# Performance work log

Measured on AMD Instinct MI355X. Metric: run time of the kernel, lower is better.

## Reference

```python
import jax, jax.numpy as jnp
import numpy as np

S1 = 2048      # seqx1_dim
S2 = 2048      # seqx2_dim
E1 = 1024      # seqx1_emb_dim
E2 = 1024      # seqx2_emb_dim
U = 1024       # units
M = E1 + E2    # margex_dim
B = 2048
TAU = 0.5


def setup_inputs() -> dict:
    key = jax.random.key(0)
    ks = jax.random.split(key, 20)
    g = lambda k, shp, fan: jax.random.normal(k, shp, jnp.float32) * (1.0 / np.sqrt(fan))
    bias = jnp.zeros((4 * U,), jnp.float32).at[U:2 * U].set(1.0)  # unit_forget_bias
    return {
        'inputs': jax.random.normal(ks[0], (B, S1 + S2), jnp.float32),
        'h_tm1': jax.random.normal(ks[1], (B, U), jnp.float32),
        'c_tm1': jax.random.normal(ks[2], (B, U), jnp.float32),
        'crohis_tm': jax.random.normal(ks[3], (B, M), jnp.float32),
        'embed_w1': g(ks[4], (S1, E1), S1),
        'embed_w2': g(ks[5], (S2, E2), S2),
        'w12_w': g(ks[6], (E1, E1), E1),
        'w12_u': g(ks[7], (E2, E1), E2),
        'w12_v': g(ks[8], (E2, E1), E2),
        'w21_w': g(ks[9], (E2, E2), E2),
        'w21_u': g(ks[10], (E1, E2), E1),
        'w21_v': g(ks[11], (E1, E2), E1),
        'crohis_w': g(ks[12], (M, U), M),
        'crohis_b': jnp.zeros((U,), jnp.float32),
        'decomp_w': g(ks[13], (M, M), M),
        'decomp_b': jnp.zeros((M,), jnp.float32),
        'kernel': g(ks[14], (M, 4 * U), M),
        'recurrent_kernel': g(ks[15], (U, 4 * U), U),
        'bias': bias,
    }


def _cell(inputs, h_tm1, c_tm1, crohis_tm, embed_w1, embed_w2, w12_w, w12_u, w12_v,
          w21_w, w21_u, w21_v, crohis_w, crohis_b, decomp_w, decomp_b,
          kernel, recurrent_kernel, bias):
    seqx1 = inputs[:, :S1]
    seqx2 = inputs[:, S1:]
    e1 = seqx1 @ embed_w1                                   # [B,E1]
    e2 = seqx2 @ embed_w2                                   # [B,E2]
    # dual cross-attention gates (softmax over feature axis, as K.softmax default)
    ca12 = jax.nn.softmax(jnp.tanh(e1 @ w12_w + e2 @ w12_u) * (e2 @ w12_v), axis=-1)
    ca21 = jax.nn.softmax(jnp.tanh(e2 @ w21_w + e1 @ w21_u) * (e1 @ w21_v), axis=-1)
    x = jnp.concatenate([e1 * ca12, e2 * ca21], axis=-1)    # [B,M]
    # cross-history decomposition gate and decayed merge
    decomp = jax.nn.sigmoid(crohis_tm @ decomp_w + decomp_b)
    crohis = TAU * crohis_tm * decomp + (1.0 - TAU) * x     # [B,M]
    h_cro = jnp.tanh(crohis @ crohis_w + crohis_b)          # [B,U]
    # fused LSTM (implementation=2)
    z = x @ kernel + h_tm1 @ recurrent_kernel + bias        # [B,4U]
    zi, zf, zc, zo = jnp.split(z, 4, axis=-1)
    i = jax.nn.sigmoid(zi)
    f = jax.nn.sigmoid(zf)
    c = f * c_tm1 + i * jnp.tanh(zc)
    o = jax.nn.sigmoid(zo)
    h = o * jnp.tanh(c) + h_cro
    return h, c, crohis


def reference(inputs, h_tm1, c_tm1, crohis_tm, embed_w1, embed_w2, w12_w, w12_u, w12_v,
              w21_w, w21_u, w21_v, crohis_w, crohis_b, decomp_w, decomp_b,
              kernel, recurrent_kernel, bias):
    return _cell(inputs, h_tm1, c_tm1, crohis_tm, embed_w1, embed_w2, w12_w, w12_u,
                 w12_v, w21_w, w21_u, w21_v, crohis_w, crohis_b, decomp_w, decomp_b,
                 kernel, recurrent_kernel, bias)
```

## Files before the change

### kernel.cpp

```cpp
#include <hip/hip_runtime.h>
#include <stdint.h>

typedef unsigned short u16;
typedef __bf16 bf16x8 __attribute__((ext_vector_type(8)));
typedef float f32x4 __attribute__((ext_vector_type(4)));
typedef u16 u16x8 __attribute__((ext_vector_type(8)));

__device__ __forceinline__ u16 bf16_bits(float f) {
  uint32_t x = __float_as_uint(f);
  uint32_t r = (x + 0x7FFFu + ((x >> 16) & 1u)) >> 16;
  return (u16)r;
}
__device__ __forceinline__ float bits_f32(u16 u) {
  return __uint_as_float(((uint32_t)u) << 16);
}
__device__ __forceinline__ float sigm(float x) { return 1.f / (1.f + expf(-x)); }

__device__ __forceinline__ void gload_lds16(const void* g, void* l) {
  __builtin_amdgcn_global_load_lds(
      (const __attribute__((address_space(1))) void*)g,
      (__attribute__((address_space(3))) void*)l,
      16, 0, 0);
}

__global__ __launch_bounds__(256) void cvt_all_kernel(
    const float* __restrict__ inp, const float* __restrict__ ctm,
    const float* __restrict__ h, u16* __restrict__ bf_in,
    u16* __restrict__ bf_ctm, u16* __restrict__ xh) {
  int i = blockIdx.x * 256 + threadIdx.x;
  const float* src;
  u16* dst;
  if (i < 1048576) {
    src = inp + (size_t)i * 8;
    dst = bf_in + (size_t)i * 8;
  } else if (i < 1048576 + 524288) {
    int j = i - 1048576;
    src = ctm + (size_t)j * 8;
    dst = bf_ctm + (size_t)j * 8;
  } else {
    int j = i - 1572864;
    int row = j >> 7;
    int c0 = (j & 127) << 3;
    src = h + (size_t)row * 1024 + c0;
    dst = xh + (size_t)row * 3072 + 2048 + c0;
  }
  const f32x4* s = (const f32x4*)src;
  f32x4 a = s[0], b = s[1];
  u16x8 o;
#pragma unroll
  for (int k = 0; k < 4; ++k) { o[k] = bf16_bits(a[k]); o[4 + k] = bf16_bits(b[k]); }
  *(u16x8*)dst = o;
}

struct TransGroups {
  const float* src[12];
  u16* dst[12];
  int N[12];
  int ld[12];
  long long off[12];
  int start[13];
};

__global__ __launch_bounds__(256) void transpose_all_kernel(TransGroups tg) {
  __shared__ float t[32][33];
  int bid = blockIdx.x;
  int g = 0;
#pragma unroll
  for (int i = 1; i < 12; ++i)
    if (bid >= tg.start[i]) g = i;
  int local = bid - tg.start[g];
  const float* src = tg.src[g];
  u16* dst = tg.dst[g];
  int N = tg.N[g];
  int ld = tg.ld[g];
  long long off = tg.off[g];
  int ntx = N >> 5;
  int n0 = (local % ntx) << 5;
  int k0 = (local / ntx) << 5;
  int tx = threadIdx.x & 31, ty = threadIdx.x >> 5;
#pragma unroll
  for (int r = ty; r < 32; r += 8) t[r][tx] = src[(size_t)(k0 + r) * N + n0 + tx];
  __syncthreads();
#pragma unroll
  for (int r = ty; r < 32; r += 8)
    dst[off + (size_t)(n0 + r) * ld + k0 + tx] = bf16_bits(t[tx][r]);
}

enum { EPI_F32 = 0, EPI_BF16 = 1, EPI_DHALF = 2, EPI_TANH = 3 };

struct GemmGroups {
  const u16* A[4];
  const u16* Bt[4];
  float* C[4];
  u16* Cb[4];
  const float* bias[4];
  const float* aux[4];
  int lda[4];
  int K[4];
  int nbx[4];
  int ldc[4];
  int ldcb[4];
  int epi[4];
  int start[4];
};

__global__ __launch_bounds__(256) void gemm_grouped(GemmGroups gg) {
  __shared__ u16 As[128 * 32];
  __shared__ u16 Bs[128 * 32];
  const int bid = blockIdx.x;
  int g = 0;
#pragma unroll
  for (int i = 1; i < 4; ++i)
    if (bid >= gg.start[i]) g = i;
  const int local = bid - gg.start[g];
  const u16* __restrict__ A = gg.A[g];
  const u16* __restrict__ Bt = gg.Bt[g];
  const int lda = gg.lda[g];
  const int K = gg.K[g];
  const int nbx = gg.nbx[g];

  const int tid = threadIdx.x;
  const int lane = tid & 63;
  const int wid = tid >> 6;
  const int wr = wid >> 1, wc = wid & 1;
  const int brow = (local / nbx) * 128;
  const int bcol = (local % nbx) * 128;

  f32x4 acc[4][4] = {};

  const int s0 = wid, s1 = wid + 4;
  const int oA0 = s0 * 1024 + lane * 16;
  const int oA1 = s1 * 1024 + lane * 16;

  const int nk = K >> 5;
  for (int kt = 0; kt < nk; ++kt) {
    __syncthreads();
    {
      const char* gp;
      int o = oA0;
      gp = (const char*)A + (((size_t)(brow + (o >> 6)) * lda) << 1) + (kt << 6) + (o & 63);
      gload_lds16(gp, (char*)As + s0 * 1024);
      o = oA1;
      gp = (const char*)A + (((size_t)(brow + (o >> 6)) * lda) << 1) + (kt << 6) + (o & 63);
      gload_lds16(gp, (char*)As + s1 * 1024);
      o = oA0;
      gp = (const char*)Bt + (((size_t)(bcol + (o >> 6)) * K) << 1) + (kt << 6) + (o & 63);
      gload_lds16(gp, (char*)Bs + s0 * 1024);
      o = oA1;
      gp = (const char*)Bt + (((size_t)(bcol + (o >> 6)) * K) << 1) + (kt << 6) + (o & 63);
      gload_lds16(gp, (char*)Bs + s1 * 1024);
    }
    __syncthreads();

    bf16x8 af[4], bf[4];
#pragma unroll
    for (int m = 0; m < 4; ++m) {
      int r = wr * 64 + m * 16 + (lane & 15);
      af[m] = *(const bf16x8*)((const char*)As + r * 64 + ((lane >> 4) << 4));
    }
#pragma unroll
    for (int n = 0; n < 4; ++n) {
      int cidx = wc * 64 + n * 16 + (lane & 15);
      bf[n] = *(const bf16x8*)((const char*)Bs + cidx * 64 + ((lane >> 4) << 4));
    }
#pragma unroll
    for (int m = 0; m < 4; ++m)
#pragma unroll
      for (int n = 0; n < 4; ++n)
        acc[m][n] = __builtin_amdgcn_mfma_f32_16x16x32_bf16(af[m], bf[n], acc[m][n], 0, 0, 0);
  }

  float* __restrict__ C = gg.C[g];
  u16* __restrict__ Cb = gg.Cb[g];
  const float* __restrict__ bias = gg.bias[g];
  const float* __restrict__ aux = gg.aux[g];
  const int ldc = gg.ldc[g];
  const int ldcb = gg.ldcb[g];
  const int epi = gg.epi[g];

  const int r0 = brow + wr * 64 + ((lane >> 4) << 2);
  const int c0 = bcol + wc * 64 + (lane & 15);
#pragma unroll
  for (int m = 0; m < 4; ++m) {
#pragma unroll
    for (int n = 0; n < 4; ++n) {
#pragma unroll
      for (int j = 0; j < 4; ++j) {
        int gr = r0 + m * 16 + j;
        int gc = c0 + n * 16;
        float v = acc[m][n][j];
        if (epi == EPI_F32) {
          C[(size_t)gr * ldc + gc] = v;
        } else if (epi == EPI_BF16) {
          Cb[(size_t)gr * ldcb + gc] = bf16_bits(v);
        } else if (epi == EPI_DHALF) {
          size_t ci = (size_t)gr * ldc + gc;
          C[ci] = 0.5f * aux[ci] * sigm(v + bias[gc]);
        } else {
          C[(size_t)gr * ldc + gc] = tanhf(v + bias[gc]);
        }
      }
    }
  }
}

__global__ __launch_bounds__(256) void softmax_cro_kernel(
    const float* __restrict__ T_ALL, const u16* __restrict__ E_B,
    const float* __restrict__ DCRO, u16* __restrict__ XH_B,
    float* __restrict__ out_cro, u16* __restrict__ CRO_B) {
  __shared__ float smx[4], sms[4];
  int row = blockIdx.x >> 1;
  int half = blockIdx.x & 1;
  const float* T = T_ALL + (size_t)row * 4096 + half * 1024;
  const float* V = T_ALL + (size_t)row * 4096 + 2048 + half * 1024;
  int tid = threadIdx.x;
  float s[4];
  float lmax = -1e30f;
#pragma unroll
  for (int i = 0; i < 4; ++i) {
    int c = tid + (i << 8);
    s[i] = tanhf(T[c]) * V[c];
    lmax = fmaxf(lmax, s[i]);
  }
#pragma unroll
  for (int o = 32; o; o >>= 1) lmax = fmaxf(lmax, __shfl_xor(lmax, o, 64));
  if ((tid & 63) == 0) smx[tid >> 6] = lmax;
  __syncthreads();
  float bmax = fmaxf(fmaxf(smx[0], smx[1]), fmaxf(smx[2], smx[3]));
  float lsum = 0.f;
#pragma unroll
  for (int i = 0; i < 4; ++i) { s[i] = expf(s[i] - bmax); lsum += s[i]; }
#pragma unroll
  for (int o = 32; o; o >>= 1) lsum += __shfl_xor(lsum, o, 64);
  if ((tid & 63) == 0) sms[tid >> 6] = lsum;
  __syncthreads();
  float inv = 1.f / (sms[0] + sms[1] + sms[2] + sms[3]);
#pragma unroll
  for (int i = 0; i < 4; ++i) {
    int c = tid + (i << 8);
    int col = half * 1024 + c;
    size_t mi = (size_t)row * 2048 + col;
    float x = bits_f32(E_B[mi]) * s[i] * inv;
    XH_B[(size_t)row * 3072 + col] = bf16_bits(x);
    float cro = DCRO[mi] + 0.5f * x;
    out_cro[mi] = cro;
    CRO_B[mi] = bf16_bits(cro);
  }
}

__global__ __launch_bounds__(256) void gates_kernel(
    const float* __restrict__ Z, const float* __restrict__ bias,
    const float* __restrict__ c_tm1, const float* __restrict__ hcro,
    float* __restrict__ out_h, float* __restrict__ out_c) {
  int i = blockIdx.x * 256 + threadIdx.x;
  int row = i >> 8;
  int u0 = (i & 255) << 2;
  const float* zr = Z + (size_t)row * 4096;
  f32x4 zi = *(const f32x4*)(zr + u0);
  f32x4 zf = *(const f32x4*)(zr + 1024 + u0);
  f32x4 zc = *(const f32x4*)(zr + 2048 + u0);
  f32x4 zo = *(const f32x4*)(zr + 3072 + u0);
  f32x4 bi = *(const f32x4*)(bias + u0);
  f32x4 bff = *(const f32x4*)(bias + 1024 + u0);
  f32x4 bc = *(const f32x4*)(bias + 2048 + u0);
  f32x4 bo = *(const f32x4*)(bias + 3072 + u0);
  f32x4 ct = *(const f32x4*)(c_tm1 + (size_t)row * 1024 + u0);
  f32x4 hc = *(const f32x4*)(hcro + (size_t)row * 1024 + u0);
  f32x4 h, c;
#pragma unroll
  for (int k = 0; k < 4; ++k) {
    float I = sigm(zi[k] + bi[k]);
    float F = sigm(zf[k] + bff[k]);
    float O = sigm(zo[k] + bo[k]);
    float cc = F * ct[k] + I * tanhf(zc[k] + bc[k]);
    c[k] = cc;
    h[k] = O * tanhf(cc) + hc[k];
  }
  *(f32x4*)(out_h + (size_t)row * 1024 + u0) = h;
  *(f32x4*)(out_c + (size_t)row * 1024 + u0) = c;
}

extern "C" void kernel_launch(void* const* d_in, const int* in_sizes, int n_in,
                              void* d_out, int out_size, void* d_ws, size_t ws_size,
                              hipStream_t stream) {
  const float* in_inputs = (const float*)d_in[0];
  const float* in_h      = (const float*)d_in[1];
  const float* in_c      = (const float*)d_in[2];
  const float* in_ctm    = (const float*)d_in[3];
  const float* w_e1      = (const float*)d_in[4];
  const float* w_e2      = (const float*)d_in[5];
  const float* w12w      = (const float*)d_in[6];
  const float* w12u      = (const float*)d_in[7];
  const float* w12v      = (const float*)d_in[8];
  const float* w21w      = (const float*)d_in[9];
  const float* w21u      = (const float*)d_in[10];
  const float* w21v      = (const float*)d_in[11];
  const float* w_cro     = (const float*)d_in[12];
  const float* b_cro     = (const float*)d_in[13];
  const float* w_dec     = (const float*)d_in[14];
  const float* b_dec     = (const float*)d_in[15];
  const float* w_k       = (const float*)d_in[16];
  const float* w_rk      = (const float*)d_in[17];
  const float* b_z       = (const float*)d_in[18];

  float* out_h   = (float*)d_out;
  float* out_c   = out_h + (size_t)2048 * 1024;
  float* out_cro = out_h + (size_t)2 * 2048 * 1024;

  char* ws = (char*)d_ws;
  size_t off = 0;
  auto alloc = [&](size_t bytes) {
    char* p = ws + off;
    off += (bytes + 255) & ~(size_t)255;
    return p;
  };
  u16* BF_IN    = (u16*)alloc((size_t)2048 * 4096 * 2);
  u16* BF_CROTM = (u16*)alloc((size_t)2048 * 2048 * 2);
  u16* E_B      = (u16*)alloc((size_t)2048 * 2048 * 2);
  float* T_ALL  = (float*)alloc((size_t)2048 * 4096 * 4);
  float* DCRO   = (float*)alloc((size_t)2048 * 2048 * 4);
  u16* XH_B     = (u16*)alloc((size_t)2048 * 3072 * 2);
  u16* CRO_B    = (u16*)alloc((size_t)2048 * 2048 * 2);
  float* HCRO   = (float*)alloc((size_t)2048 * 1024 * 4);
  u16* WT_E1    = (u16*)alloc((size_t)1024 * 2048 * 2);
  u16* WT_E2    = (u16*)alloc((size_t)1024 * 2048 * 2);
  u16* WT_T     = (u16*)alloc((size_t)2048 * 2048 * 2);
  u16* WT_V12   = (u16*)alloc((size_t)1024 * 1024 * 2);
  u16* WT_V21   = (u16*)alloc((size_t)1024 * 1024 * 2);
  u16* WT_CRO   = (u16*)alloc((size_t)1024 * 2048 * 2);
  u16* WT_DEC   = (u16*)alloc((size_t)2048 * 2048 * 2);
  u16* WT_KRK   = (u16*)alloc((size_t)4096 * 3072 * 2);
  float* Z = T_ALL;

  const int INF = 0x7fffffff;

  cvt_all_kernel<<<7168, 256, 0, stream>>>(in_inputs, in_ctm, in_h, BF_IN, BF_CROTM, XH_B);

  {
    TransGroups tg;
    int s = 0, gi = 0;
    auto add = [&](const float* src, int K, int N, u16* dst, int ld, long long dOff) {
      tg.src[gi] = src; tg.dst[gi] = dst; tg.N[gi] = N; tg.ld[gi] = ld; tg.off[gi] = dOff;
      tg.start[gi] = s; s += (K >> 5) * (N >> 5); ++gi;
    };
    add(w_e1, 2048, 1024, WT_E1, 2048, 0);
    add(w_e2, 2048, 1024, WT_E2, 2048, 0);
    add(w12w, 1024, 1024, WT_T, 2048, 0);
    add(w12u, 1024, 1024, WT_T, 2048, 1024);
    add(w21u, 1024, 1024, WT_T, 2048, (long long)1024 * 2048);
    add(w21w, 1024, 1024, WT_T, 2048, (long long)1024 * 2048 + 1024);
    add(w12v, 1024, 1024, WT_V12, 1024, 0);
    add(w21v, 1024, 1024, WT_V21, 1024, 0);
    add(w_cro, 2048, 1024, WT_CRO, 2048, 0);
    add(w_dec, 2048, 2048, WT_DEC, 2048, 0);
    add(w_k, 2048, 4096, WT_KRK, 3072, 0);
    add(w_rk, 1024, 4096, WT_KRK, 3072, 2048);
    tg.start[12] = s;
    transpose_all_kernel<<<s, 256, 0, stream>>>(tg);
  }

  auto mkgrp = [&]() {
    GemmGroups gg;
    for (int i = 0; i < 4; ++i) {
      gg.A[i] = nullptr; gg.Bt[i] = nullptr; gg.C[i] = nullptr; gg.Cb[i] = nullptr;
      gg.bias[i] = nullptr; gg.aux[i] = nullptr;
      gg.lda[i] = 0; gg.K[i] = 32; gg.nbx[i] = 1; gg.ldc[i] = 0; gg.ldcb[i] = 0;
      gg.epi[i] = EPI_F32; gg.start[i] = INF;
    }
    return gg;
  };

  {
    GemmGroups gg = mkgrp();
    gg.A[0] = BF_CROTM; gg.Bt[0] = WT_DEC; gg.lda[0] = 2048; gg.K[0] = 2048;
    gg.nbx[0] = 16; gg.C[0] = DCRO; gg.ldc[0] = 2048; gg.epi[0] = EPI_DHALF;
    gg.bias[0] = b_dec; gg.aux[0] = in_ctm; gg.start[0] = 0;
    gg.A[1] = BF_IN; gg.Bt[1] = WT_E1; gg.lda[1] = 4096; gg.K[1] = 2048;
    gg.nbx[1] = 8; gg.Cb[1] = E_B; gg.ldcb[1] = 2048; gg.epi[1] = EPI_BF16;
    gg.start[1] = 256;
    gg.A[2] = BF_IN + 2048; gg.Bt[2] = WT_E2; gg.lda[2] = 4096; gg.K[2] = 2048;
    gg.nbx[2] = 8; gg.Cb[2] = E_B + 1024; gg.ldcb[2] = 2048; gg.epi[2] = EPI_BF16;
    gg.start[2] = 384;
    gemm_grouped<<<512, 256, 0, stream>>>(gg);
  }

  {
    GemmGroups gg = mkgrp();
    gg.A[0] = E_B; gg.Bt[0] = WT_T; gg.lda[0] = 2048; gg.K[0] = 2048;
    gg.nbx[0] = 16; gg.C[0] = T_ALL; gg.ldc[0] = 4096; gg.epi[0] = EPI_F32;
    gg.start[0] = 0;
    gg.A[1] = E_B + 1024; gg.Bt[1] = WT_V12; gg.lda[1] = 2048; gg.K[1] = 1024;
    gg.nbx[1] = 8; gg.C[1] = T_ALL + 2048; gg.ldc[1] = 4096; gg.epi[1] = EPI_F32;
    gg.start[1] = 256;
    gg.A[2] = E_B; gg.Bt[2] = WT_V21; gg.lda[2] = 2048; gg.K[2] = 1024;
    gg.nbx[2] = 8; gg.C[2] = T_ALL + 3072; gg.ldc[2] = 4096; gg.epi[2] = EPI_F32;
    gg.start[2] = 384;
    gemm_grouped<<<512, 256, 0, stream>>>(gg);
  }

  softmax_cro_kernel<<<4096, 256, 0, stream>>>(T_ALL, E_B, DCRO, XH_B, out_cro, CRO_B);

  {
    GemmGroups gg = mkgrp();
    gg.A[0] = XH_B; gg.Bt[0] = WT_KRK; gg.lda[0] = 3072; gg.K[0] = 3072;
    gg.nbx[0] = 32; gg.C[0] = Z; gg.ldc[0] = 4096; gg.epi[0] = EPI_F32;
    gg.start[0] = 0;
    gg.A[1] = CRO_B; gg.Bt[1] = WT_CRO; gg.lda[1] = 2048; gg.K[1] = 2048;
    gg.nbx[1] = 8; gg.C[1] = HCRO; gg.ldc[1] = 1024; gg.epi[1] = EPI_TANH;
    gg.bias[1] = b_cro; gg.start[1] = 512;
    gemm_grouped<<<640, 256, 0, stream>>>(gg);
  }

  gates_kernel<<<2048, 256, 0, stream>>>(Z, b_z, in_c, HCRO, out_h, out_c);
}
```

Measured before the change: 519.6 us.

## Double-buffer GEMM LDS tiles and widen transpose tiles to packed bf16 stores

The grouped GEMM now uses two LDS buffers and issues the global-to-LDS loads for the next K tile before computing on the current one. This removes one barrier per iteration and lets memory latency overlap the MFMA work. The weight transpose kernel now handles 64x32 tiles and writes pairs of bf16 values as 32-bit stores, which halves the block count and widens the writes. The cost is double the LDS footprint, which may reduce occupancy, plus one redundant prefetch on the last iteration.

```diff
diff --git a/kernel.cpp b/kernel.cpp
--- a/kernel.cpp
+++ b/kernel.cpp
@@ -62,7 +62,7 @@
 };
 
 __global__ __launch_bounds__(256) void transpose_all_kernel(TransGroups tg) {
-  __shared__ float t[32][33];
+  __shared__ float t[64][33];
   int bid = blockIdx.x;
   int g = 0;
 #pragma unroll
@@ -74,16 +74,19 @@
   int N = tg.N[g];
   int ld = tg.ld[g];
   long long off = tg.off[g];
-  int ntx = N >> 5;
-  int n0 = (local % ntx) << 5;
-  int k0 = (local / ntx) << 5;
+  int ntn = N >> 5;
+  int n0 = (local % ntn) << 5;
+  int k0 = (local / ntn) << 6;
   int tx = threadIdx.x & 31, ty = threadIdx.x >> 5;
 #pragma unroll
-  for (int r = ty; r < 32; r += 8) t[r][tx] = src[(size_t)(k0 + r) * N + n0 + tx];
+  for (int r = ty; r < 64; r += 8) t[r][tx] = src[(size_t)(k0 + r) * N + n0 + tx];
   __syncthreads();
 #pragma unroll
-  for (int r = ty; r < 32; r += 8)
-    dst[off + (size_t)(n0 + r) * ld + k0 + tx] = bf16_bits(t[tx][r]);
+  for (int j = ty; j < 32; j += 8) {
+    uint32_t lo = bf16_bits(t[2 * tx][j]);
+    uint32_t hi = bf16_bits(t[2 * tx + 1][j]);
+    *(uint32_t*)(&dst[off + (size_t)(n0 + j) * ld + k0 + 2 * tx]) = lo | (hi << 16);
+  }
 }
 
 enum { EPI_F32 = 0, EPI_BF16 = 1, EPI_DHALF = 2, EPI_TANH = 3 };
@@ -105,8 +108,8 @@
 };
 
 __global__ __launch_bounds__(256) void gemm_grouped(GemmGroups gg) {
-  __shared__ u16 As[128 * 32];
-  __shared__ u16 Bs[128 * 32];
+  __shared__ u16 As[2][4096];
+  __shared__ u16 Bs[2][4096];
   const int bid = blockIdx.x;
   int g = 0;
 #pragma unroll
@@ -132,43 +135,50 @@
   const int oA0 = s0 * 1024 + lane * 16;
   const int oA1 = s1 * 1024 + lane * 16;
 
+  const char* gA0 = (const char*)A + (((size_t)(brow + (oA0 >> 6)) * lda) << 1) + (oA0 & 63);
+  const char* gA1 = (const char*)A + (((size_t)(brow + (oA1 >> 6)) * lda) << 1) + (oA1 & 63);
+  const char* gB0 = (const char*)Bt + (((size_t)(bcol + (oA0 >> 6)) * K) << 1) + (oA0 & 63);
+  const char* gB1 = (const char*)Bt + (((size_t)(bcol + (oA1 >> 6)) * K) << 1) + (oA1 & 63);
+
+#define STAGE(buf, koff)                                              \
+  {                                                                   \
+    gload_lds16(gA0 + (koff), (char*)As + (buf) * 8192 + s0 * 1024);  \
+    gload_lds16(gA1 + (koff), (char*)As + (buf) * 8192 + s1 * 1024);  \
+    gload_lds16(gB0 + (koff), (char*)Bs + (buf) * 8192 + s0 * 1024);  \
+    gload_lds16(gB1 + (koff), (char*)Bs + (buf) * 8192 + s1 * 1024);  \
+  }
+
   const int nk = K >> 5;
+  STAGE(0, 0);
+  __syncthreads();
+  int cur = 0;
   for (int kt = 0; kt < nk; ++kt) {
-    __syncthreads();
-    {
-      const char* gp;
-      int o = oA0;
-      gp = (const char*)A + (((size_t)(brow + (o >> 6)) * lda) << 1) + (kt << 6) + (o & 63);
-      gload_lds16(gp, (char*)As + s0 * 1024);
-      o = oA1;
-      gp = (const char*)A + (((size_t)(brow + (o >> 6)) * lda) << 1) + (kt << 6) + (o & 63);
-      gload_lds16(gp, (char*)As + s1 * 1024);
-      o = oA0;
-      gp = (const char*)Bt + (((size_t)(bcol + (o >> 6)) * K) << 1) + (kt << 6) + (o & 63);
-      gload_lds16(gp, (char*)Bs + s0 * 1024);
-      o = oA1;
-      gp = (const char*)Bt + (((size_t)(bcol + (o >> 6)) * K) << 1) + (kt << 6) + (o & 63);
-      gload_lds16(gp, (char*)Bs + s1 * 1024);
-    }
-    __syncthreads();
-
-    bf16x8 af[4], bf[4];
+    const int koff = (kt + 1 < nk ? kt + 1 : kt) << 6;
+    STAGE(cur ^ 1, koff);
+
+    const char* Ab = (const char*)As + cur * 8192;
+    const char* Bb = (const char*)Bs + cur * 8192;
+    bf16x8 af[4], bfr[4];
 #pragma unroll
     for (int m = 0; m < 4; ++m) {
       int r = wr * 64 + m * 16 + (lane & 15);
-      af[m] = *(const bf16x8*)((const char*)As + r * 64 + ((lane >> 4) << 4));
+      af[m] = *(const bf16x8*)(Ab + r * 64 + ((lane >> 4) << 4));
     }
 #pragma unroll
     for (int n = 0; n < 4; ++n) {
       int cidx = wc * 64 + n * 16 + (lane & 15);
-      bf[n] = *(const bf16x8*)((const char*)Bs + cidx * 64 + ((lane >> 4) << 4));
+      bfr[n] = *(const bf16x8*)(Bb + cidx * 64 + ((lane >> 4) << 4));
     }
 #pragma unroll
     for (int m = 0; m < 4; ++m)
 #pragma unroll
       for (int n = 0; n < 4; ++n)
-        acc[m][n] = __builtin_amdgcn_mfma_f32_16x16x32_bf16(af[m], bf[n], acc[m][n], 0, 0, 0);
-  }
+        acc[m][n] = __builtin_amdgcn_mfma_f32_16x16x32_bf16(af[m], bfr[n], acc[m][n], 0, 0, 0);
+
+    __syncthreads();
+    cur ^= 1;
+  }
+#undef STAGE
 
   float* __restrict__ C = gg.C[g];
   u16* __restrict__ Cb = gg.Cb[g];
@@ -341,7 +351,7 @@
     int s = 0, gi = 0;
     auto add = [&](const float* src, int K, int N, u16* dst, int ld, long long dOff) {
       tg.src[gi] = src; tg.dst[gi] = dst; tg.N[gi] = N; tg.ld[gi] = ld; tg.off[gi] = dOff;
-      tg.start[gi] = s; s += (K >> 5) * (N >> 5); ++gi;
+      tg.start[gi] = s; s += (K >> 6) * (N >> 5); ++gi;
     };
     add(w_e1, 2048, 1024, WT_E1, 2048, 0);
     add(w_e2, 2048, 1024, WT_E2, 2048, 0);
```

New measurement: 497.8 us. 4.2% less time.
